# Kernel tuning notes

Measured on AMD Instinct MI355X. Metric: run time of the kernel, lower is better.

The kernel has to match this reference:

```python
import jax, jax.numpy as jnp
import numpy as np
import math

B, SQ, SK, HEADS, DH = 4, 4096, 308, 8, 64
INNER = HEADS * DH


def setup_inputs() -> dict:
    key = jax.random.key(0)
    k1, k2, k3, k4, k5 = jax.random.split(key, 5)
    q = jax.random.normal(k1, (B, SQ, INNER), dtype=jnp.float32)
    k = jax.random.normal(k2, (B, SK, INNER), dtype=jnp.float32)
    v = jax.random.normal(k3, (B, SK, INNER), dtype=jnp.float32)
    # mask_scale: positive multiplicative rescale (H*W / mask_area in original)
    mask_scale = jax.random.uniform(k4, (B, HEADS, SQ, SK), dtype=jnp.float32) + 0.5
    # mask_bool: region membership mask (masks > 0.5 in original)
    mask_bool = jax.random.randint(k5, (B, HEADS, SQ, SK), 0, 2) > 0
    return {"q": q, "k": k, "v": v, "mask_scale": mask_scale,
            "mask_bool": mask_bool, "heads": HEADS}


def reference(q, k, v, mask_scale, mask_bool, heads):
    b, sq, inner = q.shape
    dh = inner // heads
    # (b, s, h*dh) -> (b, h, s, dh)
    def split_heads(t):
        return t.reshape(b, -1, heads, dh).transpose(0, 2, 1, 3)
    qh, kh, vh = split_heads(q), split_heads(k), split_heads(v)
    scores = jnp.einsum('bhqd,bhkd->bhqk', qh, kh) / math.sqrt(dh)
    scores = scores * mask_scale
    scores = jnp.where(mask_bool, scores, -jnp.inf)
    attn = jax.nn.softmax(scores, axis=-1)
    out = jnp.einsum('bhqk,bhkd->bhqd', attn, vh)
    # (b, h, q, dh) -> (b, q, h*dh)
    return out.transpose(0, 2, 1, 3).reshape(b, sq, heads * dh)
```

## Files before the change

### kernel.cpp

```cpp
#include <hip/hip_runtime.h>


#define NB     4
#define NSQ    4096
#define NSK    308
#define NH     8
#define NDH    64
#define NINNER 512
#define NKT    20
#define QBLK   64
#define NTHREADS 256
#define NCH    (QBLK*NSK/4)

#define KFRAG_PER_BH (NKT*2*64*8)
#define VFRAG_PER_BH (NKT*4*64*4)
#define WS_BYTES ((size_t)(NB*NH) * (KFRAG_PER_BH + VFRAG_PER_BH) * 2)

typedef _Float16 h8 __attribute__((ext_vector_type(8)));
typedef _Float16 h4 __attribute__((ext_vector_type(4)));
typedef float    f4 __attribute__((ext_vector_type(4)));
typedef int      i4 __attribute__((ext_vector_type(4)));

__global__ __launch_bounds__(512) void omost_prep(
    const float* __restrict__ Kg, const float* __restrict__ Vg,
    _Float16* __restrict__ ws)
{
  const int bh  = blockIdx.x;
  const int b   = bh >> 3;
  const int h   = bh & 7;
  const int tid = threadIdx.x;

  _Float16* Kfrag = ws + (size_t)bh * KFRAG_PER_BH;
  _Float16* Vfrag = ws + (size_t)(NB*NH) * KFRAG_PER_BH + (size_t)bh * VFRAG_PER_BH;

  const float* Kb = Kg + (size_t)b * NSK * NINNER + h * NDH;
  #pragma unroll
  for (int i = 0; i < (NKT*2*64) / 512; ++i) {
    int s   = tid + i * 512;
    int l   = s & 63;
    int dhc = (s >> 6) & 1;
    int kt  = s >> 7;
    int row = kt * 16 + (l & 15);
    int col = dhc * 32 + ((l >> 4) << 3);
    h8 hk;
    #pragma unroll
    for (int j = 0; j < 8; ++j) hk[j] = (_Float16)0.f;
    if (row < NSK) {
      const float* p = Kb + (size_t)row * NINNER + col;
      f4 a = *(const f4*)p;
      f4 c = *(const f4*)(p + 4);
      hk[0]=(_Float16)a[0]; hk[1]=(_Float16)a[1]; hk[2]=(_Float16)a[2]; hk[3]=(_Float16)a[3];
      hk[4]=(_Float16)c[0]; hk[5]=(_Float16)c[1]; hk[6]=(_Float16)c[2]; hk[7]=(_Float16)c[3];
    }
    *(h8*)(Kfrag + (size_t)s * 8) = hk;
  }

  const float* Vb = Vg + (size_t)b * NSK * NINNER + h * NDH;
  #pragma unroll
  for (int i = 0; i < (NKT*4*64) / 512; ++i) {
    int s    = tid + i * 512;
    int l    = s & 63;
    int nt   = (s >> 6) & 3;
    int kt   = s >> 8;
    int col  = nt * 16 + (l & 15);
    int row0 = kt * 16 + ((l >> 4) << 2);
    h4 hv;
    #pragma unroll
    for (int j = 0; j < 4; ++j) hv[j] = (_Float16)0.f;
    #pragma unroll
    for (int j = 0; j < 4; ++j) {
      int row = row0 + j;
      if (row < NSK) hv[j] = (_Float16)Vb[(size_t)row * NINNER + col];
    }
    *(h4*)(Vfrag + (size_t)s * 4) = hv;
  }
}

__global__ __launch_bounds__(NTHREADS, 4) void omost_attn(
    const float* __restrict__ Qg, const float* __restrict__ MSg,
    const int*   __restrict__ MBg, const _Float16* __restrict__ ws,
    float* __restrict__ Og)
{
  __shared__ __align__(16) _Float16 Mlds[QBLK * NSK];

  const int tid  = threadIdx.x;
  const int lane = tid & 63;
  const int wv   = tid >> 6;
  const int lg   = lane >> 4;
  const int lr   = lane & 15;

  const int wg = blockIdx.x;
  const int qt = wg & (NSQ / QBLK - 1);
  const int bh = wg >> 6;
  const int b  = bh >> 3;
  const int h  = bh & 7;

  const int q0   = qt * QBLK + wv * 16;
  const int qrow = q0 + lr;

  const h8* Kf = (const h8*)(ws + (size_t)bh * KFRAG_PER_BH);
  const h4* Vf = (const h4*)(ws + (size_t)(NB*NH) * KFRAG_PER_BH + (size_t)bh * VFRAG_PER_BH);

  const float* Qb = Qg + ((size_t)b * NSQ + qrow) * NINNER + h * NDH;
  f4 qraw[4];
  qraw[0] = *(const f4*)(Qb + lg * 8);
  qraw[1] = *(const f4*)(Qb + lg * 8 + 4);
  qraw[2] = *(const f4*)(Qb + 32 + lg * 8);
  qraw[3] = *(const f4*)(Qb + 32 + lg * 8 + 4);

  const size_t mbase = ((size_t)bh * NSQ + qt * QBLK) * NSK;
  #pragma unroll
  for (int g = 0; g < 4; ++g) {
    f4 msr[5]; i4 mbr[5];
    #pragma unroll
    for (int j = 0; j < 5; ++j) {
      int cc  = tid + (g * 5 + j) * NTHREADS;
      int ccl = cc < NCH ? cc : NCH - 1;
      msr[j] = *(const f4*)(MSg + mbase + 4 * (size_t)ccl);
      mbr[j] = *(const i4*)(MBg + mbase + 4 * (size_t)ccl);
    }
    #pragma unroll
    for (int j = 0; j < 5; ++j) {
      int cc = tid + (g * 5 + j) * NTHREADS;
      if (cc < NCH) {
        h4 fm;
        #pragma unroll
        for (int r = 0; r < 4; ++r)
          fm[r] = (mbr[j][r] != 0) ? (_Float16)msr[j][r] : (_Float16)0.f;
        *(h4*)(&Mlds[4 * cc]) = fm;
      }
    }
  }
  __syncthreads();

  h8 qf[2];
  #pragma unroll
  for (int dhc = 0; dhc < 2; ++dhc) {
    f4 a = qraw[dhc * 2], c = qraw[dhc * 2 + 1];
    h8 t;
    t[0]=(_Float16)(a[0]*0.125f); t[1]=(_Float16)(a[1]*0.125f);
    t[2]=(_Float16)(a[2]*0.125f); t[3]=(_Float16)(a[3]*0.125f);
    t[4]=(_Float16)(c[0]*0.125f); t[5]=(_Float16)(c[1]*0.125f);
    t[6]=(_Float16)(c[2]*0.125f); t[7]=(_Float16)(c[3]*0.125f);
    qf[dhc] = t;
  }

  const int mlrow = (wv * 16 + lr) * NSK;
  f4 acc[4];
  #pragma unroll
  for (int nt = 0; nt < 4; ++nt) acc[nt] = (f4){0.f, 0.f, 0.f, 0.f};
  float ssum = 0.f;

  #pragma unroll
  for (int kt = 0; kt < NKT; ++kt) {
    const int kb  = kt * 16 + lg * 4;
    const int kbl = kb > (NSK - 4) ? (NSK - 4) : kb;
    h4 m = *(const h4*)(&Mlds[mlrow + kbl]);

    f4 c = {0.f, 0.f, 0.f, 0.f};
    c = __builtin_amdgcn_mfma_f32_16x16x32_f16(Kf[(kt*2+0)*64 + lane], qf[0], c, 0, 0, 0);
    c = __builtin_amdgcn_mfma_f32_16x16x32_f16(Kf[(kt*2+1)*64 + lane], qf[1], c, 0, 0, 0);

    h4 pa;
    #pragma unroll
    for (int r = 0; r < 4; ++r) {
      float mf = (float)m[r];
      bool ok = (kb + r < NSK) && (mf != 0.f);
      float p = ok ? __expf(__builtin_fmaf(c[r], mf, -4.f)) : 0.f;
      ssum += p;
      pa[r] = (_Float16)p;
    }
    #pragma unroll
    for (int nt = 0; nt < 4; ++nt)
      acc[nt] = __builtin_amdgcn_mfma_f32_16x16x16f16(pa, Vf[(kt*4+nt)*64 + lane], acc[nt], 0, 0, 0);
  }

  ssum += __shfl_xor(ssum, 16, 64);
  ssum += __shfl_xor(ssum, 32, 64);
  const float inv = 1.f / ssum;

  float invr[4];
  #pragma unroll
  for (int r = 0; r < 4; ++r) invr[r] = __shfl(inv, lg * 4 + r, 64);

  float* Ob = Og + (size_t)b * NSQ * NINNER + h * NDH;
  #pragma unroll
  for (int nt = 0; nt < 4; ++nt) {
    #pragma unroll
    for (int r = 0; r < 4; ++r) {
      int qq = q0 + lg * 4 + r;
      Ob[(size_t)qq * NINNER + nt * 16 + lr] = acc[nt][r] * invr[r];
    }
  }
}

extern "C" void kernel_launch(void* const* d_in, const int* in_sizes, int n_in,
                              void* d_out, int out_size, void* d_ws, size_t ws_size,
                              hipStream_t stream) {
  const float* Qg  = (const float*)d_in[0];
  const float* Kg  = (const float*)d_in[1];
  const float* Vg  = (const float*)d_in[2];
  const float* MSg = (const float*)d_in[3];
  const int*   MBg = (const int*)d_in[4];
  float* Og = (float*)d_out;
  _Float16* ws = (_Float16*)d_ws;

  if (ws_size < WS_BYTES) return;

  omost_prep<<<dim3(NB*NH), dim3(512), 0, stream>>>(Kg, Vg, ws);

  const int nwg = NB * NH * (NSQ / QBLK);
  omost_attn<<<dim3(nwg), dim3(NTHREADS), 0, stream>>>(Qg, MSg, MBg, ws, Og);
}
```

Before: 108.0 us.

## Persistent-style workgroups staging K/V in LDS and prefetching next mask tile

Each workgroup now handles eight consecutive 64-row query tiles for one (batch, head), so the grid shrinks eightfold. K and V fragments are copied once into dynamic LDS per workgroup instead of being read from global memory per tile. While the current tile computes, the next tile's mask_scale and mask_bool and its Q rows are loaded into registers, then written to the LDS mask buffer between barriers. The aim is to overlap the dominant mask streaming with MFMA and exp work and to avoid repeated K/V fetches. In exchange, about 121 KB of LDS and larger register use limit each CU to one workgroup of four waves, which cuts latency hiding, and two barriers are added per tile.

```diff
diff --git a/kernel.cpp b/kernel.cpp
--- a/kernel.cpp
+++ b/kernel.cpp
@@ -8,13 +8,19 @@
 #define NDH    64
 #define NINNER 512
 #define NKT    20
-#define QBLK   64
+#define TROWS  64
+#define NTILES 8
+#define SUPER  (NTILES*TROWS)
 #define NTHREADS 256
-#define NCH    (QBLK*NSK/4)
+#define NCH    (TROWS*NSK/4)
+#define MTILE  (TROWS*NSK)
 
 #define KFRAG_PER_BH (NKT*2*64*8)
 #define VFRAG_PER_BH (NKT*4*64*4)
 #define WS_BYTES ((size_t)(NB*NH) * (KFRAG_PER_BH + VFRAG_PER_BH) * 2)
+
+#define LDS_F16   (KFRAG_PER_BH + VFRAG_PER_BH + MTILE)
+#define LDS_BYTES (LDS_F16 * 2)
 
 typedef _Float16 h8 __attribute__((ext_vector_type(8)));
 typedef _Float16 h4 __attribute__((ext_vector_type(4)));
@@ -76,12 +82,15 @@
   }
 }
 
-__global__ __launch_bounds__(NTHREADS, 4) void omost_attn(
+__global__ __launch_bounds__(NTHREADS) void omost_attn(
     const float* __restrict__ Qg, const float* __restrict__ MSg,
     const int*   __restrict__ MBg, const _Float16* __restrict__ ws,
     float* __restrict__ Og)
 {
-  __shared__ __align__(16) _Float16 Mlds[QBLK * NSK];
+  extern __shared__ __align__(16) _Float16 smem[];
+  _Float16* Klds = smem;
+  _Float16* Vlds = smem + KFRAG_PER_BH;
+  _Float16* Mbuf = smem + KFRAG_PER_BH + VFRAG_PER_BH;
 
   const int tid  = threadIdx.x;
   const int lane = tid & 63;
@@ -89,108 +98,168 @@
   const int lg   = lane >> 4;
   const int lr   = lane & 15;
 
-  const int wg = blockIdx.x;
-  const int qt = wg & (NSQ / QBLK - 1);
-  const int bh = wg >> 6;
-  const int b  = bh >> 3;
-  const int h  = bh & 7;
-
-  const int q0   = qt * QBLK + wv * 16;
-  const int qrow = q0 + lr;
-
-  const h8* Kf = (const h8*)(ws + (size_t)bh * KFRAG_PER_BH);
-  const h4* Vf = (const h4*)(ws + (size_t)(NB*NH) * KFRAG_PER_BH + (size_t)bh * VFRAG_PER_BH);
-
-  const float* Qb = Qg + ((size_t)b * NSQ + qrow) * NINNER + h * NDH;
-  f4 qraw[4];
-  qraw[0] = *(const f4*)(Qb + lg * 8);
-  qraw[1] = *(const f4*)(Qb + lg * 8 + 4);
-  qraw[2] = *(const f4*)(Qb + 32 + lg * 8);
-  qraw[3] = *(const f4*)(Qb + 32 + lg * 8 + 4);
-
-  const size_t mbase = ((size_t)bh * NSQ + qt * QBLK) * NSK;
-  #pragma unroll
-  for (int g = 0; g < 4; ++g) {
-    f4 msr[5]; i4 mbr[5];
-    #pragma unroll
-    for (int j = 0; j < 5; ++j) {
-      int cc  = tid + (g * 5 + j) * NTHREADS;
-      int ccl = cc < NCH ? cc : NCH - 1;
-      msr[j] = *(const f4*)(MSg + mbase + 4 * (size_t)ccl);
-      mbr[j] = *(const i4*)(MBg + mbase + 4 * (size_t)ccl);
-    }
-    #pragma unroll
-    for (int j = 0; j < 5; ++j) {
-      int cc = tid + (g * 5 + j) * NTHREADS;
-      if (cc < NCH) {
-        h4 fm;
-        #pragma unroll
-        for (int r = 0; r < 4; ++r)
-          fm[r] = (mbr[j][r] != 0) ? (_Float16)msr[j][r] : (_Float16)0.f;
-        *(h4*)(&Mlds[4 * cc]) = fm;
-      }
-    }
+  const int wg    = blockIdx.x;
+  const int sup   = wg & (NSQ / SUPER - 1);
+  const int bh    = wg >> 3;
+  const int b     = bh >> 3;
+  const int h     = bh & 7;
+  const int qbase = sup * SUPER;
+
+  const h8* KfG = (const h8*)(ws + (size_t)bh * KFRAG_PER_BH);
+  const h8* VfG = (const h8*)(ws + (size_t)(NB*NH) * KFRAG_PER_BH + (size_t)bh * VFRAG_PER_BH);
+  #pragma unroll
+  for (int i = 0; i < (KFRAG_PER_BH/8) / NTHREADS; ++i)
+    ((h8*)Klds)[tid + i * NTHREADS] = KfG[tid + i * NTHREADS];
+  #pragma unroll
+  for (int i = 0; i < (VFRAG_PER_BH/8) / NTHREADS; ++i)
+    ((h8*)Vlds)[tid + i * NTHREADS] = VfG[tid + i * NTHREADS];
+
+  {
+    const size_t mb0 = ((size_t)bh * NSQ + qbase) * NSK;
+    #pragma unroll
+    for (int g = 0; g < 4; ++g) {
+      f4 msr[5]; i4 mbr[5];
+      #pragma unroll
+      for (int j = 0; j < 5; ++j) {
+        int cc  = tid + (g * 5 + j) * NTHREADS;
+        int ccl = cc < NCH ? cc : NCH - 1;
+        msr[j] = *(const f4*)(MSg + mb0 + 4 * (size_t)ccl);
+        mbr[j] = *(const i4*)(MBg + mb0 + 4 * (size_t)ccl);
+      }
+      #pragma unroll
+      for (int j = 0; j < 5; ++j) {
+        int cc = tid + (g * 5 + j) * NTHREADS;
+        if (cc < NCH) {
+          h4 fmw;
+          #pragma unroll
+          for (int r = 0; r < 4; ++r)
+            fmw[r] = (mbr[j][r] != 0) ? (_Float16)msr[j][r] : (_Float16)0.f;
+          *(h4*)(&Mbuf[4 * cc]) = fmw;
+        }
+      }
+    }
+  }
+
+  f4 qc0, qc1, qc2, qc3;
+  {
+    const float* Qb = Qg + ((size_t)b * NSQ + (qbase + wv * 16 + lr)) * NINNER + h * NDH;
+    qc0 = *(const f4*)(Qb + lg * 8);      qc1 = *(const f4*)(Qb + lg * 8 + 4);
+    qc2 = *(const f4*)(Qb + 32 + lg * 8); qc3 = *(const f4*)(Qb + 32 + lg * 8 + 4);
   }
   __syncthreads();
 
-  h8 qf[2];
-  #pragma unroll
-  for (int dhc = 0; dhc < 2; ++dhc) {
-    f4 a = qraw[dhc * 2], c = qraw[dhc * 2 + 1];
-    h8 t;
-    t[0]=(_Float16)(a[0]*0.125f); t[1]=(_Float16)(a[1]*0.125f);
-    t[2]=(_Float16)(a[2]*0.125f); t[3]=(_Float16)(a[3]*0.125f);
-    t[4]=(_Float16)(c[0]*0.125f); t[5]=(_Float16)(c[1]*0.125f);
-    t[6]=(_Float16)(c[2]*0.125f); t[7]=(_Float16)(c[3]*0.125f);
-    qf[dhc] = t;
-  }
-
+  const h8* Kf = (const h8*)Klds;
+  const h4* Vf = (const h4*)Vlds;
   const int mlrow = (wv * 16 + lr) * NSK;
-  f4 acc[4];
-  #pragma unroll
-  for (int nt = 0; nt < 4; ++nt) acc[nt] = (f4){0.f, 0.f, 0.f, 0.f};
-  float ssum = 0.f;
-
-  #pragma unroll
-  for (int kt = 0; kt < NKT; ++kt) {
-    const int kb  = kt * 16 + lg * 4;
-    const int kbl = kb > (NSK - 4) ? (NSK - 4) : kb;
-    h4 m = *(const h4*)(&Mlds[mlrow + kbl]);
-
-    f4 c = {0.f, 0.f, 0.f, 0.f};
-    c = __builtin_amdgcn_mfma_f32_16x16x32_f16(Kf[(kt*2+0)*64 + lane], qf[0], c, 0, 0, 0);
-    c = __builtin_amdgcn_mfma_f32_16x16x32_f16(Kf[(kt*2+1)*64 + lane], qf[1], c, 0, 0, 0);
-
-    h4 pa;
-    #pragma unroll
-    for (int r = 0; r < 4; ++r) {
-      float mf = (float)m[r];
-      bool ok = (kb + r < NSK) && (mf != 0.f);
-      float p = ok ? __expf(__builtin_fmaf(c[r], mf, -4.f)) : 0.f;
-      ssum += p;
-      pa[r] = (_Float16)p;
-    }
-    #pragma unroll
-    for (int nt = 0; nt < 4; ++nt)
-      acc[nt] = __builtin_amdgcn_mfma_f32_16x16x16f16(pa, Vf[(kt*4+nt)*64 + lane], acc[nt], 0, 0, 0);
-  }
-
-  ssum += __shfl_xor(ssum, 16, 64);
-  ssum += __shfl_xor(ssum, 32, 64);
-  const float inv = 1.f / ssum;
-
-  float invr[4];
-  #pragma unroll
-  for (int r = 0; r < 4; ++r) invr[r] = __shfl(inv, lg * 4 + r, 64);
-
   float* Ob = Og + (size_t)b * NSQ * NINNER + h * NDH;
-  #pragma unroll
-  for (int nt = 0; nt < 4; ++nt) {
-    #pragma unroll
-    for (int r = 0; r < 4; ++r) {
-      int qq = q0 + lg * 4 + r;
-      Ob[(size_t)qq * NINNER + nt * 16 + lr] = acc[nt][r] * invr[r];
-    }
+
+  #pragma unroll 1
+  for (int t = 0; t < NTILES; ++t) {
+    const bool more = (t < NTILES - 1);
+    const size_t mbN = ((size_t)bh * NSQ + qbase + (size_t)(t + 1) * TROWS) * NSK;
+
+    f4 qn0, qn1, qn2, qn3;
+    if (more) {
+      const float* Qb = Qg + ((size_t)b * NSQ + (qbase + (t + 1) * TROWS + wv * 16 + lr)) * NINNER + h * NDH;
+      qn0 = *(const f4*)(Qb + lg * 8);      qn1 = *(const f4*)(Qb + lg * 8 + 4);
+      qn2 = *(const f4*)(Qb + 32 + lg * 8); qn3 = *(const f4*)(Qb + 32 + lg * 8 + 4);
+    }
+
+    h8 qf[2];
+    {
+      h8 t0, t1;
+      t0[0]=(_Float16)(qc0[0]*0.125f); t0[1]=(_Float16)(qc0[1]*0.125f);
+      t0[2]=(_Float16)(qc0[2]*0.125f); t0[3]=(_Float16)(qc0[3]*0.125f);
+      t0[4]=(_Float16)(qc1[0]*0.125f); t0[5]=(_Float16)(qc1[1]*0.125f);
+      t0[6]=(_Float16)(qc1[2]*0.125f); t0[7]=(_Float16)(qc1[3]*0.125f);
+      t1[0]=(_Float16)(qc2[0]*0.125f); t1[1]=(_Float16)(qc2[1]*0.125f);
+      t1[2]=(_Float16)(qc2[2]*0.125f); t1[3]=(_Float16)(qc2[3]*0.125f);
+      t1[4]=(_Float16)(qc3[0]*0.125f); t1[5]=(_Float16)(qc3[1]*0.125f);
+      t1[6]=(_Float16)(qc3[2]*0.125f); t1[7]=(_Float16)(qc3[3]*0.125f);
+      qf[0] = t0; qf[1] = t1;
+    }
+
+    h4 fm[20];
+    f4 acc[4];
+    #pragma unroll
+    for (int nt = 0; nt < 4; ++nt) acc[nt] = (f4){0.f, 0.f, 0.f, 0.f};
+    float ssum = 0.f;
+
+    #pragma unroll
+    for (int g = 0; g < 4; ++g) {
+      f4 msr[5]; i4 mbr[5];
+      if (more) {
+        #pragma unroll
+        for (int j = 0; j < 5; ++j) {
+          int cc  = tid + (g * 5 + j) * NTHREADS;
+          int ccl = cc < NCH ? cc : NCH - 1;
+          msr[j] = *(const f4*)(MSg + mbN + 4 * (size_t)ccl);
+          mbr[j] = *(const i4*)(MBg + mbN + 4 * (size_t)ccl);
+        }
+      }
+      #pragma unroll
+      for (int k5 = 0; k5 < 5; ++k5) {
+        const int kt  = g * 5 + k5;
+        const int kb  = kt * 16 + lg * 4;
+        const int kbl = kb > (NSK - 4) ? (NSK - 4) : kb;
+        h4 m = *(const h4*)(&Mbuf[mlrow + kbl]);
+
+        f4 c = {0.f, 0.f, 0.f, 0.f};
+        c = __builtin_amdgcn_mfma_f32_16x16x32_f16(Kf[(kt*2+0)*64 + lane], qf[0], c, 0, 0, 0);
+        c = __builtin_amdgcn_mfma_f32_16x16x32_f16(Kf[(kt*2+1)*64 + lane], qf[1], c, 0, 0, 0);
+
+        h4 pa;
+        #pragma unroll
+        for (int r = 0; r < 4; ++r) {
+          float mf = (float)m[r];
+          bool ok = (kb + r < NSK) && (mf != 0.f);
+          float p = ok ? __expf(__builtin_fmaf(c[r], mf, -4.f)) : 0.f;
+          ssum += p;
+          pa[r] = (_Float16)p;
+        }
+        #pragma unroll
+        for (int nt = 0; nt < 4; ++nt)
+          acc[nt] = __builtin_amdgcn_mfma_f32_16x16x16f16(pa, Vf[(kt*4+nt)*64 + lane], acc[nt], 0, 0, 0);
+      }
+      if (more) {
+        #pragma unroll
+        for (int j = 0; j < 5; ++j) {
+          h4 fmw;
+          #pragma unroll
+          for (int r = 0; r < 4; ++r)
+            fmw[r] = (mbr[j][r] != 0) ? (_Float16)msr[j][r] : (_Float16)0.f;
+          fm[g * 5 + j] = fmw;
+        }
+      }
+    }
+
+    ssum += __shfl_xor(ssum, 16, 64);
+    ssum += __shfl_xor(ssum, 32, 64);
+    const float inv = 1.f / fmaxf(ssum, 1e-30f);
+    float invr[4];
+    #pragma unroll
+    for (int r = 0; r < 4; ++r) invr[r] = __shfl(inv, lg * 4 + r, 64);
+
+    const int q0t = qbase + t * TROWS + wv * 16;
+    #pragma unroll
+    for (int nt = 0; nt < 4; ++nt) {
+      #pragma unroll
+      for (int r = 0; r < 4; ++r) {
+        int qq = q0t + lg * 4 + r;
+        Ob[(size_t)qq * NINNER + nt * 16 + lr] = acc[nt][r] * invr[r];
+      }
+    }
+
+    __syncthreads();
+    if (more) {
+      #pragma unroll
+      for (int s5 = 0; s5 < 20; ++s5) {
+        int cc = tid + s5 * NTHREADS;
+        if (cc < NCH) *(h4*)(&Mbuf[4 * cc]) = fm[s5];
+      }
+      qc0 = qn0; qc1 = qn1; qc2 = qn2; qc3 = qn3;
+    }
+    __syncthreads();
   }
 }
 
@@ -207,8 +276,12 @@
 
   if (ws_size < WS_BYTES) return;
 
+  static_assert(LDS_BYTES <= 160 * 1024, "exceeds gfx950 LDS");
+  (void)hipFuncSetAttribute((const void*)omost_attn,
+                            hipFuncAttributeMaxDynamicSharedMemorySize, LDS_BYTES);
+
   omost_prep<<<dim3(NB*NH), dim3(512), 0, stream>>>(Kg, Vg, ws);
 
-  const int nwg = NB * NH * (NSQ / QBLK);
-  omost_attn<<<dim3(nwg), dim3(NTHREADS), 0, stream>>>(Qg, MSg, MBg, ws, Og);
+  const int nwg = NB * NH * (NSQ / SUPER);
+  omost_attn<<<dim3(nwg), dim3(NTHREADS), LDS_BYTES, stream>>>(Qg, MSg, MBg, ws, Og);
 }
```

New measurement: 103.9 us. 1.04x faster.
